# Performance work log

Hardware: AMD Instinct MI355X
Metric: run time of the kernel (lower is better)

## Reference

```python
import jax, jax.numpy as jnp
from jax import lax
import numpy as np

C = 256       # residual_channels == skip_channels
B = 4
T = 4096
LATENT = 128
NB = 4        # n_blocks
NL = 10       # n_layers
ENC_DILS = tuple(2 ** i for i in range(NL)) * NB   # 40 encoder blocks
DEC_DILS = tuple(2 ** i for i in range(NL))        # 10 decoder blocks


def causal_conv(x, W, b, d):
    # x: [B, Cin, T], W: [Cout, Cin, k], left-pad by (k-1)*d for causality
    pad = (W.shape[-1] - 1) * d
    y = lax.conv_general_dilated(x, W, (1,), [(pad, 0)], rhs_dilation=(d,),
                                 dimension_numbers=('NCH', 'OIH', 'NCH'))
    return y + b[None, :, None]


def gated_block(h, Wf, bf, Wg, bg, Wr, br, Ws, bs, d):
    f = jnp.tanh(causal_conv(h, Wf, bf, d))
    g = jax.nn.sigmoid(causal_conv(h, Wg, bg, d))
    out = f * g
    res = jnp.einsum('oc,bct->bot', Wr, out) + br[None, :, None] + h
    skip = jnp.einsum('oc,bct->bot', Ws, out) + bs[None, :, None]
    return res, skip


def setup_inputs() -> dict:
    key = jax.random.key(0)
    ks = jax.random.split(key, 24)
    s = 0.05
    nE = NB * NL
    d = {}
    d['x'] = jax.random.normal(ks[0], (B, 1, T), jnp.float32)
    d['eps'] = jax.random.normal(ks[1], (B, LATENT), jnp.float32)
    d['enc_in_W'] = jax.random.normal(ks[2], (C, 1, 2)) * s
    d['enc_in_b'] = jnp.zeros((C,), jnp.float32)
    d['enc_Wf'] = jax.random.normal(ks[3], (nE, C, C, 2)) * s
    d['enc_bf'] = jnp.zeros((nE, C), jnp.float32)
    d['enc_Wg'] = jax.random.normal(ks[4], (nE, C, C, 2)) * s
    d['enc_bg'] = jnp.zeros((nE, C), jnp.float32)
    d['enc_Wr'] = jax.random.normal(ks[5], (nE, C, C)) * s
    d['enc_br'] = jnp.zeros((nE, C), jnp.float32)
    d['enc_Ws'] = jax.random.normal(ks[6], (nE, C, C)) * s
    d['enc_bs'] = jnp.zeros((nE, C), jnp.float32)
    d['fc_mu_W'] = jax.random.normal(ks[7], (LATENT, C)) * s
    d['fc_mu_b'] = jnp.zeros((LATENT,), jnp.float32)
    d['fc_lv_W'] = jax.random.normal(ks[8], (LATENT, C)) * s
    d['fc_lv_b'] = jnp.zeros((LATENT,), jnp.float32)
    d['dec_in_W'] = jax.random.normal(ks[9], (C, LATENT)) * s
    d['dec_in_b'] = jnp.zeros((C,), jnp.float32)
    d['dec_Wf'] = jax.random.normal(ks[10], (NL, C, C, 2)) * s
    d['dec_bf'] = jnp.zeros((NL, C), jnp.float32)
    d['dec_Wg'] = jax.random.normal(ks[11], (NL, C, C, 2)) * s
    d['dec_bg'] = jnp.zeros((NL, C), jnp.float32)
    d['dec_Wr'] = jax.random.normal(ks[12], (NL, C, C)) * s
    d['dec_br'] = jnp.zeros((NL, C), jnp.float32)
    d['out_W'] = jax.random.normal(ks[13], (1, C)) * s
    d['out_b'] = jnp.zeros((1,), jnp.float32)
    return d


def _forward(x, eps, enc_in_W, enc_in_b, enc_Wf, enc_bf, enc_Wg, enc_bg,
             enc_Wr, enc_br, enc_Ws, enc_bs, fc_mu_W, fc_mu_b, fc_lv_W, fc_lv_b,
             dec_in_W, dec_in_b, dec_Wf, dec_bf, dec_Wg, dec_bg, dec_Wr, dec_br,
             out_W, out_b):
    # --- encode ---
    h = causal_conv(x, enc_in_W, enc_in_b, 1)
    skip_sum = jnp.zeros((h.shape[0], C, h.shape[2]), h.dtype)
    for i, dil in enumerate(ENC_DILS):
        h, skip = gated_block(h, enc_Wf[i], enc_bf[i], enc_Wg[i], enc_bg[i],
                              enc_Wr[i], enc_br[i], enc_Ws[i], enc_bs[i], dil)
        skip_sum = skip_sum + skip
    pooled = skip_sum.mean(axis=-1)                      # [B, C]
    mu = pooled @ fc_mu_W.T + fc_mu_b                    # [B, LATENT]
    logvar = pooled @ fc_lv_W.T + fc_lv_b
    # --- reparameterize ---
    z = mu + eps * jnp.exp(0.5 * logvar)
    # --- decode (length-1 sequence) ---
    h2 = (jnp.einsum('ol,bl->bo', dec_in_W, z) + dec_in_b)[:, :, None]  # [B, C, 1]
    for i, dil in enumerate(DEC_DILS):
        f = jnp.tanh(causal_conv(h2, dec_Wf[i], dec_bf[i], dil))
        g = jax.nn.sigmoid(causal_conv(h2, dec_Wg[i], dec_bg[i], dil))
        out = f * g
        h2 = jnp.einsum('oc,bct->bot', dec_Wr[i], out) + dec_br[i][None, :, None] + h2
    y = jnp.einsum('oc,bct->bot', out_W, h2) + out_b[None, :, None]     # [B, 1, 1]
    return (y, mu, logvar)


def reference(x, eps, enc_in_W, enc_in_b, enc_Wf, enc_bf, enc_Wg, enc_bg,
              enc_Wr, enc_br, enc_Ws, enc_bs, fc_mu_W, fc_mu_b, fc_lv_W, fc_lv_b,
              dec_in_W, dec_in_b, dec_Wf, dec_bf, dec_Wg, dec_bg, dec_Wr, dec_br,
              out_W, out_b):
    return _forward(x, eps, enc_in_W, enc_in_b, enc_Wf, enc_bf, enc_Wg, enc_bg,
                    enc_Wr, enc_br, enc_Ws, enc_bs, fc_mu_W, fc_mu_b, fc_lv_W, fc_lv_b,
                    dec_in_W, dec_in_b, dec_Wf, dec_bf, dec_Wg, dec_bg, dec_Wr, dec_br,
                    out_W, out_b)
```

## Files before the change

kernel.cpp:

```cpp
#include <hip/hip_runtime.h>

typedef unsigned short u16;
typedef __attribute__((ext_vector_type(8))) __bf16 bf16x8;
typedef __attribute__((ext_vector_type(4))) float f32x4;

constexpr int C = 256;
constexpr int T = 4096;
constexpr int B = 4;
constexpr int NENC = 40;
constexpr int NDEC = 10;
constexpr int TILE = 64;

__device__ __forceinline__ float bf2f(u16 v) {
  union { unsigned u; float f; } x;
  x.u = ((unsigned)v) << 16;
  return x.f;
}
__device__ __forceinline__ u16 f2bf(float f) {
  union { float ff; unsigned u; } x;
  x.ff = f;
  unsigned r = x.u + 0x7fffu + ((x.u >> 16) & 1u);
  return (u16)(r >> 16);
}
__device__ __forceinline__ int swz(int row, int col) {
  int g = ((row & 7) ^ (row >> 3)) & 7;
  return row * 512 + (col ^ (g << 3));
}

typedef __attribute__((address_space(1))) const unsigned int* gp1_t;
typedef __attribute__((address_space(3))) unsigned int* lp3_t;
__device__ __forceinline__ void gl_lds16(const u16* g, u16* l) {
  __builtin_amdgcn_global_load_lds((gp1_t)(const void*)g, (lp3_t)(void*)l, 16, 0, 0);
}

__global__ void k_pack1(const float* __restrict__ Wf, const float* __restrict__ Wg,
                        u16* __restrict__ penc1, int total) {
  int p = blockIdx.x * 256 + threadIdx.x;
  if (p >= total) return;
  int lane = p & 63;
  int s = (p >> 6) & 3;
  int c = (p >> 8) & 15;
  int wv = (p >> 12) & 7;
  int layer = p >> 15;
  int co = wv * 32 + (s & 1) * 16 + (lane & 15);
  int k = c * 32 + (lane >> 4) * 8;
  const float* src = (s >= 2 ? Wg : Wf) + ((size_t)layer * C + co) * 512 + k;
  u16* dst = penc1 + (size_t)p * 8;
#pragma unroll
  for (int r = 0; r < 8; ++r) dst[r] = f2bf(src[r]);
}

__global__ void k_pack2(const float* __restrict__ Wr, u16* __restrict__ penc2, int total) {
  int p = blockIdx.x * 256 + threadIdx.x;
  if (p >= total) return;
  int lane = p & 63;
  int s = (p >> 6) & 1;
  int c = (p >> 7) & 7;
  int wv = (p >> 10) & 7;
  int layer = p >> 13;
  int co = wv * 32 + s * 16 + (lane & 15);
  int k = c * 32 + (lane >> 4) * 8;
  const float* src = Wr + ((size_t)layer * C + co) * 256 + k;
  u16* dst = penc2 + (size_t)p * 8;
#pragma unroll
  for (int r = 0; r < 8; ++r) dst[r] = f2bf(src[r]);
}

__global__ void k_packd(const float* __restrict__ dWf, const float* __restrict__ dWg,
                        const float* __restrict__ dWr, const float* __restrict__ dinW,
                        u16* __restrict__ pdfg, u16* __restrict__ pdr,
                        u16* __restrict__ tdin) {
  int p = blockIdx.x * 256 + threadIdx.x;
  if (p < 163840) {
    int lane = p & 63;
    int s = (p >> 6) & 1;
    int c = (p >> 7) & 7;
    int wv = (p >> 10) & 15;
    int layer = p >> 14;
    int co = wv * 16 + (lane & 15);
    int k = c * 32 + (lane >> 4) * 8;
    const float* src = (s ? dWg : dWf) + (((size_t)(layer * C + co)) * C + k) * 2 + 1;
    u16* dst = pdfg + (size_t)p * 8;
#pragma unroll
    for (int r = 0; r < 8; ++r) dst[r] = f2bf(src[2 * r]);
  } else if (p < 245760) {
    int q = p - 163840;
    int lane = q & 63;
    int c = (q >> 6) & 7;
    int wv = (q >> 9) & 15;
    int layer = q >> 13;
    int co = wv * 16 + (lane & 15);
    int k = c * 32 + (lane >> 4) * 8;
    const float* src = dWr + ((size_t)(layer * C + co)) * C + k;
    u16* dst = pdr + (size_t)q * 8;
#pragma unroll
    for (int r = 0; r < 8; ++r) dst[r] = f2bf(src[r]);
  } else if (p < 249856) {
    int u = p - 245760;
#pragma unroll
    for (int r = 0; r < 8; ++r) tdin[u * 8 + r] = f2bf(dinW[u * 8 + r]);
  }
}

__global__ void k_zero(float* __restrict__ p, int n) {
  int i = blockIdx.x * 256 + threadIdx.x;
  if (i < n) p[i] = 0.f;
}

__global__ void k_input(const float* __restrict__ x, const float* __restrict__ W,
                        const float* __restrict__ bin, float* __restrict__ h) {
  int idx = blockIdx.x * 256 + threadIdx.x;
  int t = idx & (T - 1);
  int c = (idx >> 12) & (C - 1);
  int b = idx >> 20;
  float xv = x[b * T + t];
  float xp = (t > 0) ? x[b * T + t - 1] : 0.f;
  h[idx] = W[2 * c] * xp + W[2 * c + 1] * xv + bin[c];
}

__global__ __launch_bounds__(512, 2) void k_enc(
    const float* __restrict__ hin, float* __restrict__ hout, float* __restrict__ rowsum_l,
    const u16* __restrict__ pw1, const float* __restrict__ bfb,
    const float* __restrict__ bgb,
    const u16* __restrict__ pw2, const float* __restrict__ brb,
    int dil) {
  extern __shared__ __align__(16) u16 smem[];
  u16* wb = smem + 64 * 512;
  const int tid = threadIdx.x;
  const int wave = tid >> 6;
  const int lane = tid & 63;
  const int ncol = lane & 15;
  const int quad = lane >> 4;
  const int wg = blockIdx.x;
  const int b = wg >> 6;
  const int t0 = (wg & 63) * TILE;
  const float* hb = hin + b * C * T;

  const int co0 = wave * 32;
  const int kq = quad * 8;
  const u16* b1 = pw1 + wave * 32768 + lane * 8;
  const u16* b2 = pw2 + wave * 8192 + lane * 8;
  u16* wreg0 = wb + wave * 2048;
  u16* wreg1 = wb + 16384 + wave * 2048;
  const int aoff = lane * 8;

#pragma unroll
  for (int cc = 0; cc < 2; ++cc) {
    u16* ld = cc ? wreg1 : wreg0;
    gl_lds16(b1 + cc * 2048, ld);
    gl_lds16(b1 + cc * 2048 + 512, ld + 512);
    gl_lds16(b1 + cc * 2048 + 1024, ld + 1024);
    gl_lds16(b1 + cc * 2048 + 1536, ld + 1536);
  }

  const int n4 = tid & 15;
  const int cib = tid >> 4;
  float4 v[16];
  const bool al4 = ((dil & 3) == 0);
  if (t0 >= dil) {
#pragma unroll
    for (int it2 = 0; it2 < 16; ++it2) {
      int ci = (cib + it2 * 32) & 255;
      int tap = it2 >> 3;
      int tb = t0 + n4 * 4 - (tap ? 0 : dil);
      const float* p = hb + ci * T + tb;
      if (tap || al4) {
        v[it2] = *(const float4*)p;
      } else {
        v[it2].x = p[0]; v[it2].y = p[1]; v[it2].z = p[2]; v[it2].w = p[3];
      }
    }
  } else {
#pragma unroll
    for (int it2 = 0; it2 < 16; ++it2) {
      int ci = (cib + it2 * 32) & 255;
      int tap = it2 >> 3;
      int tb = t0 + n4 * 4 - (tap ? 0 : dil);
      const float* p = hb + ci * T + tb;
      if (tap) {
        v[it2] = *(const float4*)p;
      } else {
        v[it2].x = (tb + 0 >= 0) ? p[0] : 0.f;
        v[it2].y = (tb + 1 >= 0) ? p[1] : 0.f;
        v[it2].z = (tb + 2 >= 0) ? p[2] : 0.f;
        v[it2].w = (tb + 3 >= 0) ? p[3] : 0.f;
      }
    }
  }
#pragma unroll
  for (int it2 = 0; it2 < 8; ++it2) {
    int ci = (cib + it2 * 32) & 255;
    const float* p0 = (const float*)&v[it2];
    const float* p1 = (const float*)&v[it2 + 8];
#pragma unroll
    for (int r = 0; r < 4; ++r) {
      unsigned w32 = (unsigned)f2bf(p0[r]) | ((unsigned)f2bf(p1[r]) << 16);
      *(unsigned*)(&smem[swz(n4 * 4 + r, 2 * ci)]) = w32;
    }
  }
  __syncthreads();

  f32x4 acc[4][4];
#pragma unroll
  for (int m = 0; m < 4; ++m)
#pragma unroll
    for (int nt = 0; nt < 4; ++nt)
      acc[m][nt] = (f32x4){0.f, 0.f, 0.f, 0.f};

#pragma unroll
  for (int c = 0; c < 16; ++c) {
    if (c < 15) asm volatile("s_waitcnt vmcnt(4)" ::: "memory");
    else        asm volatile("s_waitcnt vmcnt(0)" ::: "memory");
    const u16* wr_ = (c & 1) ? wreg1 : wreg0;
    bf16x8 af0 = *(const bf16x8*)(wr_ + aoff);
    bf16x8 af1 = *(const bf16x8*)(wr_ + 512 + aoff);
    bf16x8 af2 = *(const bf16x8*)(wr_ + 1024 + aoff);
    bf16x8 af3 = *(const bf16x8*)(wr_ + 1536 + aoff);
    const int kk = c * 32 + kq;
    bf16x8 bfr[4];
#pragma unroll
    for (int nt = 0; nt < 4; ++nt)
      bfr[nt] = *(const bf16x8*)(&smem[swz(nt * 16 + ncol, kk)]);
#pragma unroll
    for (int nt = 0; nt < 4; ++nt) {
      acc[0][nt] = __builtin_amdgcn_mfma_f32_16x16x32_bf16(af0, bfr[nt], acc[0][nt], 0, 0, 0);
      acc[1][nt] = __builtin_amdgcn_mfma_f32_16x16x32_bf16(af1, bfr[nt], acc[1][nt], 0, 0, 0);
      acc[2][nt] = __builtin_amdgcn_mfma_f32_16x16x32_bf16(af2, bfr[nt], acc[2][nt], 0, 0, 0);
      acc[3][nt] = __builtin_amdgcn_mfma_f32_16x16x32_bf16(af3, bfr[nt], acc[3][nt], 0, 0, 0);
    }
    if (c + 2 < 16) {
      asm volatile("s_waitcnt lgkmcnt(0)" ::: "memory");
      u16* ld = (c & 1) ? wreg1 : wreg0;
      const u16* gs = b1 + (c + 2) * 2048;
      gl_lds16(gs, ld);
      gl_lds16(gs + 512, ld + 512);
      gl_lds16(gs + 1024, ld + 1024);
      gl_lds16(gs + 1536, ld + 1536);
    }
  }

#pragma unroll
  for (int cc = 0; cc < 2; ++cc) {
    u16* ld = cc ? wreg1 : wreg0;
    gl_lds16(b2 + cc * 1024, ld);
    gl_lds16(b2 + cc * 1024 + 512, ld + 512);
  }
  __syncthreads();

  float* rsb = rowsum_l + b * C;
#pragma unroll
  for (int j = 0; j < 2; ++j) {
    const int cob = co0 + j * 16 + quad * 4;
    float bfv[4], bgv[4], rs[4];
#pragma unroll
    for (int r = 0; r < 4; ++r) {
      bfv[r] = bfb[cob + r];
      bgv[r] = bgb[cob + r];
      rs[r] = 0.f;
    }
#pragma unroll
    for (int nt = 0; nt < 4; ++nt) {
      const int n = nt * 16 + ncol;
      u16 pk[4];
#pragma unroll
      for (int r = 0; r < 4; ++r) {
        float fv = acc[j][nt][r] + bfv[r];
        float gv = acc[2 + j][nt][r] + bgv[r];
        float th = 1.f - 2.f / (__expf(2.f * fv) + 1.f);
        float sg = 1.f / (1.f + __expf(-gv));
        float o = th * sg;
        rs[r] += o;
        pk[r] = f2bf(o);
      }
      uint2 w;
      w.x = (unsigned)pk[0] | ((unsigned)pk[1] << 16);
      w.y = (unsigned)pk[2] | ((unsigned)pk[3] << 16);
      *(uint2*)(&smem[swz(n, cob)]) = w;
    }
#pragma unroll
    for (int r = 0; r < 4; ++r) {
      float s = rs[r];
      s += __shfl_xor(s, 1);
      s += __shfl_xor(s, 2);
      s += __shfl_xor(s, 4);
      s += __shfl_xor(s, 8);
      if (ncol == 0) atomicAdd(&rsb[cob + r], s);
    }
  }
  __syncthreads();

  f32x4 acc2[2][4];
#pragma unroll
  for (int m = 0; m < 2; ++m)
#pragma unroll
    for (int nt = 0; nt < 4; ++nt)
      acc2[m][nt] = (f32x4){0.f, 0.f, 0.f, 0.f};

#pragma unroll
  for (int c = 0; c < 8; ++c) {
    if (c < 7) asm volatile("s_waitcnt vmcnt(2)" ::: "memory");
    else       asm volatile("s_waitcnt vmcnt(0)" ::: "memory");
    const u16* wr_ = (c & 1) ? wreg1 : wreg0;
    bf16x8 af0 = *(const bf16x8*)(wr_ + aoff);
    bf16x8 af1 = *(const bf16x8*)(wr_ + 512 + aoff);
    const int kk = c * 32 + kq;
    bf16x8 bfr[4];
#pragma unroll
    for (int nt = 0; nt < 4; ++nt)
      bfr[nt] = *(const bf16x8*)(&smem[swz(nt * 16 + ncol, kk)]);
#pragma unroll
    for (int nt = 0; nt < 4; ++nt) {
      acc2[0][nt] = __builtin_amdgcn_mfma_f32_16x16x32_bf16(af0, bfr[nt], acc2[0][nt], 0, 0, 0);
      acc2[1][nt] = __builtin_amdgcn_mfma_f32_16x16x32_bf16(af1, bfr[nt], acc2[1][nt], 0, 0, 0);
    }
    if (c + 2 < 8) {
      asm volatile("s_waitcnt lgkmcnt(0)" ::: "memory");
      u16* ld = (c & 1) ? wreg1 : wreg0;
      const u16* gs = b2 + (c + 2) * 1024;
      gl_lds16(gs, ld);
      gl_lds16(gs + 512, ld + 512);
    }
  }
  __syncthreads();

  float* fb = (float*)smem;
#pragma unroll
  for (int m = 0; m < 2; ++m) {
    const int cob = co0 + m * 16 + quad * 4;
#pragma unroll
    for (int nt = 0; nt < 4; ++nt) {
      const int t = nt * 16 + ncol;
#pragma unroll
      for (int r = 0; r < 4; ++r)
        fb[(cob + r) * 66 + t] = acc2[m][nt][r] + brb[cob + r];
    }
  }
  __syncthreads();
  float* ho = hout + b * C * T;
#pragma unroll
  for (int it2 = 0; it2 < 8; ++it2) {
    const int ci = cib + it2 * 32;
    const float* fr = fb + ci * 66 + n4 * 4;
    float4 o;
    o.x = fr[0] + v[it2 + 8].x;
    o.y = fr[1] + v[it2 + 8].y;
    o.z = fr[2] + v[it2 + 8].z;
    o.w = fr[3] + v[it2 + 8].w;
    *(float4*)(ho + ci * T + t0 + n4 * 4) = o;
  }
}

__global__ __launch_bounds__(256) void k_skip(
    const float* __restrict__ encWs, const float* __restrict__ encbs,
    const float* __restrict__ rowsum, float* __restrict__ pooled) {
  __shared__ float rs[B][C];
  const int l = blockIdx.x;
  const int co = threadIdx.x;
  for (int i = co; i < B * C; i += 256) rs[i >> 8][i & 255] = rowsum[l * B * C + i];
  __syncthreads();
  const float* Wrow = encWs + (size_t)l * C * C + co * C;
  float bs = encbs[l * C + co] * (float)T;
  float d[B] = {0.f, 0.f, 0.f, 0.f};
  for (int ci = 0; ci < C; ci += 4) {
    float4 w = *(const float4*)(Wrow + ci);
#pragma unroll
    for (int b = 0; b < B; ++b)
      d[b] += w.x * rs[b][ci] + w.y * rs[b][ci + 1] + w.z * rs[b][ci + 2] + w.w * rs[b][ci + 3];
  }
#pragma unroll
  for (int b = 0; b < B; ++b) atomicAdd(&pooled[b * C + co], d[b] + bs);
}

__global__ __launch_bounds__(256) void k_fc(
    const float* __restrict__ pooled,
    const float* __restrict__ muW, const float* __restrict__ mub,
    const float* __restrict__ lvW, const float* __restrict__ lvb,
    float* __restrict__ mlbuf, float* __restrict__ dout) {
  __shared__ float pm[B * C];
  const int tid = threadIdx.x;
  for (int i = tid; i < B * C; i += 256) pm[i] = pooled[i] * (1.f / (float)T);
  __syncthreads();
  const int waveG = blockIdx.x * 4 + (tid >> 6);
  const int lane = tid & 63;
  for (int j = 0; j < 16; ++j) {
    int d = waveG * 16 + j;
    int b = d >> 8, r = d & 255, which = r >> 7, l = r & 127;
    const float* Wrow = (which ? lvW : muW) + l * C;
    const float* p = pm + b * C;
    float s = Wrow[lane] * p[lane] + Wrow[lane + 64] * p[lane + 64] +
              Wrow[lane + 128] * p[lane + 128] + Wrow[lane + 192] * p[lane + 192];
#pragma unroll
    for (int off = 32; off; off >>= 1) s += __shfl_xor(s, off);
    if (lane == 0) {
      float val = s + (which ? lvb[l] : mub[l]);
      mlbuf[which * 512 + b * 128 + l] = val;
      dout[4 + which * 512 + b * 128 + l] = val;
    }
  }
}

__global__ __launch_bounds__(1024, 1) void k_dec(
    const float* __restrict__ mlbuf, const float* __restrict__ eps,
    const u16* __restrict__ tdin, const float* __restrict__ dinb,
    const u16* __restrict__ pdfg, const float* __restrict__ dbf,
    const float* __restrict__ dbg,
    const u16* __restrict__ pdr, const float* __restrict__ dbr,
    const float* __restrict__ outW, const float* __restrict__ outb,
    float* __restrict__ dout) {
  extern __shared__ __align__(16) u16 dsm[];
  __shared__ __align__(16) u16 Ah[16][264];
  __shared__ __align__(16) u16 Ao[16][264];
  __shared__ float h2f[4][256];
  __shared__ float outred[4];
  const int tid = threadIdx.x;
  const int wave = tid >> 6;
  const int lane = tid & 63;
  const int ncol = lane & 15;
  const int quad = lane >> 4;
  const int kq = quad * 8;
  const int co = wave * 16 + ncol;
  u16* wreg = dsm + wave * 4096;

  bf16x8 tdw[4];
  {
    const u16* wp = tdin + co * 128;
#pragma unroll
    for (int it = 0; it < 4; ++it) tdw[it] = *(const bf16x8*)(wp + it * 32 + kq);
  }

  if (tid < 512) {
    int b = tid >> 7, l = tid & 127;
    float mu = mlbuf[b * 128 + l];
    float lv = mlbuf[512 + b * 128 + l];
    Ah[b][l] = f2bf(mu + eps[b * 128 + l] * expf(0.5f * lv));
  }
  if (tid < 4) outred[tid] = 0.f;
  __syncthreads();

  {
    f32x4 acch = (f32x4){0.f, 0.f, 0.f, 0.f};
#pragma unroll
    for (int it = 0; it < 4; ++it) {
      bf16x8 af = *(const bf16x8*)(&Ah[ncol][it * 32 + kq]);
      acch = __builtin_amdgcn_mfma_f32_16x16x32_bf16(af, tdw[it], acch, 0, 0, 0);
    }
    __syncthreads();
    if (quad == 0) {
      float bias = dinb[co];
#pragma unroll
      for (int r = 0; r < 4; ++r) {
        float hv = acch[r] + bias;
        h2f[r][co] = hv;
        Ah[r][co] = f2bf(hv);
      }
    }
  }
  {
    const u16* fb = pdfg + wave * 8192 + lane * 8;
#pragma unroll
    for (int cc = 0; cc < 4; ++cc) {
      gl_lds16(fb + cc * 1024, wreg + cc * 1024);
      gl_lds16(fb + cc * 1024 + 512, wreg + cc * 1024 + 512);
    }
  }
  __syncthreads();

  for (int i = 0; i < NDEC; ++i) {
    const u16* fb = pdfg + (i * 16 + wave) * 8192 + lane * 8;
    const u16* rb = pdr + (i * 16 + wave) * 4096 + lane * 8;

    f32x4 accf = (f32x4){0.f, 0.f, 0.f, 0.f};
    f32x4 accg = (f32x4){0.f, 0.f, 0.f, 0.f};
#pragma unroll
    for (int c = 0; c < 8; ++c) {
      if (c == 4) asm volatile("s_waitcnt vmcnt(6)" ::: "memory");
      else if (c == 5) asm volatile("s_waitcnt vmcnt(4)" ::: "memory");
      else if (c == 6) asm volatile("s_waitcnt vmcnt(2)" ::: "memory");
      else if (c == 7) asm volatile("s_waitcnt vmcnt(0)" ::: "memory");
      const u16* bufp = wreg + (c & 3) * 1024;
      bf16x8 bf_ = *(const bf16x8*)(bufp + lane * 8);
      bf16x8 bg_ = *(const bf16x8*)(bufp + 512 + lane * 8);
      bf16x8 af = *(const bf16x8*)(&Ah[ncol][c * 32 + kq]);
      accf = __builtin_amdgcn_mfma_f32_16x16x32_bf16(af, bf_, accf, 0, 0, 0);
      accg = __builtin_amdgcn_mfma_f32_16x16x32_bf16(af, bg_, accg, 0, 0, 0);
      if (c < 4) {
        asm volatile("s_waitcnt lgkmcnt(0)" ::: "memory");
        gl_lds16(fb + (c + 4) * 1024, wreg + (c & 3) * 1024);
        gl_lds16(fb + (c + 4) * 1024 + 512, wreg + (c & 3) * 1024 + 512);
      }
    }
    asm volatile("s_waitcnt lgkmcnt(0)" ::: "memory");
#pragma unroll
    for (int cc = 0; cc < 4; ++cc) gl_lds16(rb + cc * 512, wreg + cc * 1024);

    if (quad == 0) {
      float bfv = dbf[i * C + co];
      float bgv = dbg[i * C + co];
#pragma unroll
      for (int r = 0; r < 4; ++r) {
        float fv = accf[r] + bfv;
        float gv = accg[r] + bgv;
        float th = 1.f - 2.f / (__expf(2.f * fv) + 1.f);
        float sg = 1.f / (1.f + __expf(-gv));
        Ao[r][co] = f2bf(th * sg);
      }
    }
    __syncthreads();

    f32x4 accr = (f32x4){0.f, 0.f, 0.f, 0.f};
#pragma unroll
    for (int c = 0; c < 8; ++c) {
      if (c == 4) asm volatile("s_waitcnt vmcnt(3)" ::: "memory");
      else if (c == 5) asm volatile("s_waitcnt vmcnt(2)" ::: "memory");
      else if (c == 6) asm volatile("s_waitcnt vmcnt(1)" ::: "memory");
      else if (c == 7) asm volatile("s_waitcnt vmcnt(0)" ::: "memory");
      bf16x8 br_ = *(const bf16x8*)(wreg + (c & 3) * 1024 + lane * 8);
      bf16x8 af = *(const bf16x8*)(&Ao[ncol][c * 32 + kq]);
      accr = __builtin_amdgcn_mfma_f32_16x16x32_bf16(af, br_, accr, 0, 0, 0);
      if (c < 4) {
        asm volatile("s_waitcnt lgkmcnt(0)" ::: "memory");
        gl_lds16(rb + (c + 4) * 512, wreg + (c & 3) * 1024);
      }
    }
    if (i + 1 < NDEC) {
      const u16* nfb = pdfg + ((i + 1) * 16 + wave) * 8192 + lane * 8;
      asm volatile("s_waitcnt lgkmcnt(0)" ::: "memory");
#pragma unroll
      for (int cc = 0; cc < 4; ++cc) {
        gl_lds16(nfb + cc * 1024, wreg + cc * 1024);
        gl_lds16(nfb + cc * 1024 + 512, wreg + cc * 1024 + 512);
      }
    }
    if (quad == 0) {
      float brv = dbr[i * C + co];
#pragma unroll
      for (int r = 0; r < 4; ++r) {
        float hv = h2f[r][co] + accr[r] + brv;
        h2f[r][co] = hv;
        Ah[r][co] = f2bf(hv);
      }
    }
    __syncthreads();
  }

  {
    int b = tid >> 8, c = tid & 255;
    float val = outW[c] * h2f[b][c];
#pragma unroll
    for (int off = 32; off; off >>= 1) val += __shfl_xor(val, off);
    if (lane == 0) atomicAdd(&outred[b], val);
  }
  __syncthreads();
  if (tid < 4) dout[tid] = outred[tid] + outb[0];
}

extern "C" void kernel_launch(void* const* d_in, const int* in_sizes, int n_in,
                              void* d_out, int out_size, void* d_ws, size_t ws_size,
                              hipStream_t stream) {
  const float* x      = (const float*)d_in[0];
  const float* eps    = (const float*)d_in[1];
  const float* encinW = (const float*)d_in[2];
  const float* encinb = (const float*)d_in[3];
  const float* encWf  = (const float*)d_in[4];
  const float* encbf  = (const float*)d_in[5];
  const float* encWg  = (const float*)d_in[6];
  const float* encbg  = (const float*)d_in[7];
  const float* encWr  = (const float*)d_in[8];
  const float* encbr  = (const float*)d_in[9];
  const float* encWs  = (const float*)d_in[10];
  const float* encbs  = (const float*)d_in[11];
  const float* muW    = (const float*)d_in[12];
  const float* mub    = (const float*)d_in[13];
  const float* lvW    = (const float*)d_in[14];
  const float* lvb    = (const float*)d_in[15];
  const float* dinW   = (const float*)d_in[16];
  const float* dinb   = (const float*)d_in[17];
  const float* dWf    = (const float*)d_in[18];
  const float* dbf    = (const float*)d_in[19];
  const float* dWg    = (const float*)d_in[20];
  const float* dbg    = (const float*)d_in[21];
  const float* dWr    = (const float*)d_in[22];
  const float* dbr    = (const float*)d_in[23];
  const float* outW   = (const float*)d_in[24];
  const float* outb   = (const float*)d_in[25];
  float* dout = (float*)d_out;

  char* ws = (char*)d_ws;
  float* hA = (float*)ws;
  float* hB = hA + (size_t)B * C * T;
  float* pooled = hB + (size_t)B * C * T;
  float* mlbuf = pooled + B * C;
  float* rowsum = mlbuf + 1024;
  u16* penc1 = (u16*)(rowsum + NENC * B * C);
  u16* penc2 = penc1 + (size_t)10485760;
  u16* pdfg = penc2 + (size_t)2621440;
  u16* pdr = pdfg + (size_t)1310720;
  u16* tdin = pdr + (size_t)655360;

  (void)hipFuncSetAttribute(reinterpret_cast<const void*>(k_enc),
                            hipFuncAttributeMaxDynamicSharedMemorySize, 131072);
  (void)hipFuncSetAttribute(reinterpret_cast<const void*>(k_dec),
                            hipFuncAttributeMaxDynamicSharedMemorySize, 131072);

  k_pack1<<<(1310720 + 255) / 256, 256, 0, stream>>>(encWf, encWg, penc1, 1310720);
  k_pack2<<<(327680 + 255) / 256, 256, 0, stream>>>(encWr, penc2, 327680);
  k_packd<<<(249856 + 255) / 256, 256, 0, stream>>>(dWf, dWg, dWr, dinW, pdfg, pdr, tdin);

  const int nZ = B * C + 1024 + NENC * B * C;
  k_zero<<<(nZ + 255) / 256, 256, 0, stream>>>(pooled, nZ);
  k_input<<<(B * C * T) / 256, 256, 0, stream>>>(x, encinW, encinb, hA);

  for (int i = 0; i < NENC; ++i) {
    const int dil = 1 << (i % 10);
    const float* hi = (i & 1) ? hB : hA;
    float* ho = (i & 1) ? hA : hB;
    k_enc<<<256, 512, 131072, stream>>>(
        hi, ho, rowsum + (size_t)i * B * C,
        penc1 + (size_t)i * 262144, encbf + (size_t)i * C,
        encbg + (size_t)i * C,
        penc2 + (size_t)i * 65536, encbr + (size_t)i * C,
        dil);
  }

  k_skip<<<NENC, 256, 0, stream>>>(encWs, encbs, rowsum, pooled);
  k_fc<<<16, 256, 0, stream>>>(pooled, muW, mub, lvW, lvb, mlbuf, dout);
  k_dec<<<1, 1024, 131072, stream>>>(mlbuf, eps, tdin, dinb, pdfg, dbf, dbg,
                                     pdr, dbr, outW, outb, dout);
}
```

Before: 1.279 ms.

## Use 1024-thread encoder blocks with 16 waves and triple-buffered weight streaming

Each encoder workgroup now runs 16 waves instead of 8, so every wave owns 16 output channels rather than 32. The weight packing layout is regenerated to match, and the per-wave weight staging moves from double to triple buffering in LDS. The activation tile is stored as half-width slabs, written in two phases with extra barriers partway through the K loop. This aims to raise latency hiding per CU and cut per-wave register pressure. The cost is more barriers and smaller per-wave MFMA tiles, which means less reuse of each B fragment.

```diff
diff --git a/kernel.cpp b/kernel.cpp
--- a/kernel.cpp
+++ b/kernel.cpp
@@ -22,9 +22,9 @@
   unsigned r = x.u + 0x7fffu + ((x.u >> 16) & 1u);
   return (u16)(r >> 16);
 }
-__device__ __forceinline__ int swz(int row, int col) {
+__device__ __forceinline__ int swz2(int row, int col) {
   int g = ((row & 7) ^ (row >> 3)) & 7;
-  return row * 512 + (col ^ (g << 3));
+  return row * 256 + (col ^ (g << 3));
 }
 
 typedef __attribute__((address_space(1))) const unsigned int* gp1_t;
@@ -38,13 +38,13 @@
   int p = blockIdx.x * 256 + threadIdx.x;
   if (p >= total) return;
   int lane = p & 63;
-  int s = (p >> 6) & 3;
-  int c = (p >> 8) & 15;
-  int wv = (p >> 12) & 7;
+  int s = (p >> 6) & 1;
+  int chunk = (p >> 7) & 15;
+  int w = (p >> 11) & 15;
   int layer = p >> 15;
-  int co = wv * 32 + (s & 1) * 16 + (lane & 15);
-  int k = c * 32 + (lane >> 4) * 8;
-  const float* src = (s >= 2 ? Wg : Wf) + ((size_t)layer * C + co) * 512 + k;
+  int co = w * 16 + (lane & 15);
+  int k = chunk * 32 + (lane >> 4) * 8;
+  const float* src = (s ? Wg : Wf) + ((size_t)layer * C + co) * 512 + k;
   u16* dst = penc1 + (size_t)p * 8;
 #pragma unroll
   for (int r = 0; r < 8; ++r) dst[r] = f2bf(src[r]);
@@ -54,12 +54,11 @@
   int p = blockIdx.x * 256 + threadIdx.x;
   if (p >= total) return;
   int lane = p & 63;
-  int s = (p >> 6) & 1;
-  int c = (p >> 7) & 7;
-  int wv = (p >> 10) & 7;
+  int chunk = (p >> 6) & 7;
+  int w = (p >> 9) & 15;
   int layer = p >> 13;
-  int co = wv * 32 + s * 16 + (lane & 15);
-  int k = c * 32 + (lane >> 4) * 8;
+  int co = w * 16 + (lane & 15);
+  int k = chunk * 32 + (lane >> 4) * 8;
   const float* src = Wr + ((size_t)layer * C + co) * 256 + k;
   u16* dst = penc2 + (size_t)p * 8;
 #pragma unroll
@@ -118,139 +117,129 @@
   h[idx] = W[2 * c] * xp + W[2 * c + 1] * xv + bin[c];
 }
 
-__global__ __launch_bounds__(512, 2) void k_enc(
+__global__ __launch_bounds__(1024, 1) void k_enc(
     const float* __restrict__ hin, float* __restrict__ hout, float* __restrict__ rowsum_l,
     const u16* __restrict__ pw1, const float* __restrict__ bfb,
     const float* __restrict__ bgb,
     const u16* __restrict__ pw2, const float* __restrict__ brb,
     int dil) {
   extern __shared__ __align__(16) u16 smem[];
-  u16* wb = smem + 64 * 512;
+  u16* wb = smem + 16384;
   const int tid = threadIdx.x;
   const int wave = tid >> 6;
   const int lane = tid & 63;
   const int ncol = lane & 15;
   const int quad = lane >> 4;
+  const int kq = quad * 8;
   const int wg = blockIdx.x;
   const int b = wg >> 6;
   const int t0 = (wg & 63) * TILE;
   const float* hb = hin + b * C * T;
 
-  const int co0 = wave * 32;
-  const int kq = quad * 8;
-  const u16* b1 = pw1 + wave * 32768 + lane * 8;
-  const u16* b2 = pw2 + wave * 8192 + lane * 8;
-  u16* wreg0 = wb + wave * 2048;
-  u16* wreg1 = wb + 16384 + wave * 2048;
-  const int aoff = lane * 8;
-
-#pragma unroll
-  for (int cc = 0; cc < 2; ++cc) {
-    u16* ld = cc ? wreg1 : wreg0;
-    gl_lds16(b1 + cc * 2048, ld);
-    gl_lds16(b1 + cc * 2048 + 512, ld + 512);
-    gl_lds16(b1 + cc * 2048 + 1024, ld + 1024);
-    gl_lds16(b1 + cc * 2048 + 1536, ld + 1536);
+  const u16* b1 = pw1 + wave * 16384 + lane * 8;
+  const u16* b2 = pw2 + wave * 4096 + lane * 8;
+  u16* wreg = wb + wave * 3072;
+
+#pragma unroll
+  for (int q = 0; q < 3; ++q) {
+    gl_lds16(b1 + q * 1024, wreg + q * 1024);
+    gl_lds16(b1 + q * 1024 + 512, wreg + q * 1024 + 512);
   }
 
   const int n4 = tid & 15;
-  const int cib = tid >> 4;
-  float4 v[16];
+  const int cib = (tid >> 4) & 63;
+  float4 v[8];
   const bool al4 = ((dil & 3) == 0);
   if (t0 >= dil) {
 #pragma unroll
-    for (int it2 = 0; it2 < 16; ++it2) {
-      int ci = (cib + it2 * 32) & 255;
-      int tap = it2 >> 3;
-      int tb = t0 + n4 * 4 - (tap ? 0 : dil);
-      const float* p = hb + ci * T + tb;
-      if (tap || al4) {
-        v[it2] = *(const float4*)p;
-      } else {
-        v[it2].x = p[0]; v[it2].y = p[1]; v[it2].z = p[2]; v[it2].w = p[3];
-      }
+    for (int j = 0; j < 4; ++j) {
+      int ci = cib + j * 64;
+      const float* p0 = hb + ci * T + t0 + n4 * 4 - dil;
+      if (al4) v[j] = *(const float4*)p0;
+      else { v[j].x = p0[0]; v[j].y = p0[1]; v[j].z = p0[2]; v[j].w = p0[3]; }
+      v[4 + j] = *(const float4*)(hb + ci * T + t0 + n4 * 4);
     }
   } else {
 #pragma unroll
-    for (int it2 = 0; it2 < 16; ++it2) {
-      int ci = (cib + it2 * 32) & 255;
-      int tap = it2 >> 3;
-      int tb = t0 + n4 * 4 - (tap ? 0 : dil);
-      const float* p = hb + ci * T + tb;
-      if (tap) {
-        v[it2] = *(const float4*)p;
-      } else {
-        v[it2].x = (tb + 0 >= 0) ? p[0] : 0.f;
-        v[it2].y = (tb + 1 >= 0) ? p[1] : 0.f;
-        v[it2].z = (tb + 2 >= 0) ? p[2] : 0.f;
-        v[it2].w = (tb + 3 >= 0) ? p[3] : 0.f;
-      }
-    }
-  }
-#pragma unroll
-  for (int it2 = 0; it2 < 8; ++it2) {
-    int ci = (cib + it2 * 32) & 255;
-    const float* p0 = (const float*)&v[it2];
-    const float* p1 = (const float*)&v[it2 + 8];
+    for (int j = 0; j < 4; ++j) {
+      int ci = cib + j * 64;
+      int tb = t0 + n4 * 4 - dil;
+      const float* p0 = hb + ci * T + tb;
+      v[j].x = (tb + 0 >= 0) ? p0[0] : 0.f;
+      v[j].y = (tb + 1 >= 0) ? p0[1] : 0.f;
+      v[j].z = (tb + 2 >= 0) ? p0[2] : 0.f;
+      v[j].w = (tb + 3 >= 0) ? p0[3] : 0.f;
+      v[4 + j] = *(const float4*)(hb + ci * T + t0 + n4 * 4);
+    }
+  }
+#pragma unroll
+  for (int j = 0; j < 2; ++j) {
+    int lc = 2 * cib + 128 * (j & 1);
+    const float* pa = (const float*)&v[j];
+    const float* pb = (const float*)&v[4 + j];
 #pragma unroll
     for (int r = 0; r < 4; ++r) {
-      unsigned w32 = (unsigned)f2bf(p0[r]) | ((unsigned)f2bf(p1[r]) << 16);
-      *(unsigned*)(&smem[swz(n4 * 4 + r, 2 * ci)]) = w32;
-    }
-  }
-  __syncthreads();
-
-  f32x4 acc[4][4];
-#pragma unroll
-  for (int m = 0; m < 4; ++m)
+      unsigned w32 = (unsigned)f2bf(pa[r]) | ((unsigned)f2bf(pb[r]) << 16);
+      *(unsigned*)(&smem[swz2(n4 * 4 + r, lc)]) = w32;
+    }
+  }
+  __syncthreads();
+
+  f32x4 accF[4], accG[4];
+#pragma unroll
+  for (int nt = 0; nt < 4; ++nt) {
+    accF[nt] = (f32x4){0.f, 0.f, 0.f, 0.f};
+    accG[nt] = (f32x4){0.f, 0.f, 0.f, 0.f};
+  }
+
+#pragma unroll
+  for (int gc = 0; gc < 16; ++gc) {
+    if (gc == 8) {
+      __syncthreads();
+#pragma unroll
+      for (int j = 2; j < 4; ++j) {
+        int lc = 2 * cib + 128 * (j & 1);
+        const float* pa = (const float*)&v[j];
+        const float* pb = (const float*)&v[4 + j];
+#pragma unroll
+        for (int r = 0; r < 4; ++r) {
+          unsigned w32 = (unsigned)f2bf(pa[r]) | ((unsigned)f2bf(pb[r]) << 16);
+          *(unsigned*)(&smem[swz2(n4 * 4 + r, lc)]) = w32;
+        }
+      }
+      __syncthreads();
+    }
+    if (gc <= 13)      asm volatile("s_waitcnt vmcnt(4)" ::: "memory");
+    else if (gc == 14) asm volatile("s_waitcnt vmcnt(2)" ::: "memory");
+    else               asm volatile("s_waitcnt vmcnt(0)" ::: "memory");
+    const u16* bufp = wreg + (gc % 3) * 1024;
+    bf16x8 af = *(const bf16x8*)(bufp + lane * 8);
+    bf16x8 ag = *(const bf16x8*)(bufp + 512 + lane * 8);
+    const int lc = (gc & 7) * 32 + kq;
+    bf16x8 bfr[4];
 #pragma unroll
     for (int nt = 0; nt < 4; ++nt)
-      acc[m][nt] = (f32x4){0.f, 0.f, 0.f, 0.f};
-
-#pragma unroll
-  for (int c = 0; c < 16; ++c) {
-    if (c < 15) asm volatile("s_waitcnt vmcnt(4)" ::: "memory");
-    else        asm volatile("s_waitcnt vmcnt(0)" ::: "memory");
-    const u16* wr_ = (c & 1) ? wreg1 : wreg0;
-    bf16x8 af0 = *(const bf16x8*)(wr_ + aoff);
-    bf16x8 af1 = *(const bf16x8*)(wr_ + 512 + aoff);
-    bf16x8 af2 = *(const bf16x8*)(wr_ + 1024 + aoff);
-    bf16x8 af3 = *(const bf16x8*)(wr_ + 1536 + aoff);
-    const int kk = c * 32 + kq;
-    bf16x8 bfr[4];
-#pragma unroll
-    for (int nt = 0; nt < 4; ++nt)
-      bfr[nt] = *(const bf16x8*)(&smem[swz(nt * 16 + ncol, kk)]);
+      bfr[nt] = *(const bf16x8*)(&smem[swz2(nt * 16 + ncol, lc)]);
 #pragma unroll
     for (int nt = 0; nt < 4; ++nt) {
-      acc[0][nt] = __builtin_amdgcn_mfma_f32_16x16x32_bf16(af0, bfr[nt], acc[0][nt], 0, 0, 0);
-      acc[1][nt] = __builtin_amdgcn_mfma_f32_16x16x32_bf16(af1, bfr[nt], acc[1][nt], 0, 0, 0);
-      acc[2][nt] = __builtin_amdgcn_mfma_f32_16x16x32_bf16(af2, bfr[nt], acc[2][nt], 0, 0, 0);
-      acc[3][nt] = __builtin_amdgcn_mfma_f32_16x16x32_bf16(af3, bfr[nt], acc[3][nt], 0, 0, 0);
-    }
-    if (c + 2 < 16) {
+      accF[nt] = __builtin_amdgcn_mfma_f32_16x16x32_bf16(af, bfr[nt], accF[nt], 0, 0, 0);
+      accG[nt] = __builtin_amdgcn_mfma_f32_16x16x32_bf16(ag, bfr[nt], accG[nt], 0, 0, 0);
+    }
+    if (gc + 3 < 16) {
       asm volatile("s_waitcnt lgkmcnt(0)" ::: "memory");
-      u16* ld = (c & 1) ? wreg1 : wreg0;
-      const u16* gs = b1 + (c + 2) * 2048;
-      gl_lds16(gs, ld);
-      gl_lds16(gs + 512, ld + 512);
-      gl_lds16(gs + 1024, ld + 1024);
-      gl_lds16(gs + 1536, ld + 1536);
-    }
-  }
-
-#pragma unroll
-  for (int cc = 0; cc < 2; ++cc) {
-    u16* ld = cc ? wreg1 : wreg0;
-    gl_lds16(b2 + cc * 1024, ld);
-    gl_lds16(b2 + cc * 1024 + 512, ld + 512);
-  }
+      u16* ld = wreg + (gc % 3) * 1024;
+      gl_lds16(b1 + (gc + 3) * 1024, ld);
+      gl_lds16(b1 + (gc + 3) * 1024 + 512, ld + 512);
+    }
+  }
+
+#pragma unroll
+  for (int q = 0; q < 3; ++q) gl_lds16(b2 + q * 512, wreg + q * 1024);
   __syncthreads();
 
   float* rsb = rowsum_l + b * C;
-#pragma unroll
-  for (int j = 0; j < 2; ++j) {
-    const int cob = co0 + j * 16 + quad * 4;
+  {
+    const int cob = wave * 16 + quad * 4;
     float bfv[4], bgv[4], rs[4];
 #pragma unroll
     for (int r = 0; r < 4; ++r) {
@@ -260,12 +249,12 @@
     }
 #pragma unroll
     for (int nt = 0; nt < 4; ++nt) {
-      const int n = nt * 16 + ncol;
+      const int t = nt * 16 + ncol;
       u16 pk[4];
 #pragma unroll
       for (int r = 0; r < 4; ++r) {
-        float fv = acc[j][nt][r] + bfv[r];
-        float gv = acc[2 + j][nt][r] + bgv[r];
+        float fv = accF[nt][r] + bfv[r];
+        float gv = accG[nt][r] + bgv[r];
         float th = 1.f - 2.f / (__expf(2.f * fv) + 1.f);
         float sg = 1.f / (1.f + __expf(-gv));
         float o = th * sg;
@@ -275,7 +264,7 @@
       uint2 w;
       w.x = (unsigned)pk[0] | ((unsigned)pk[1] << 16);
       w.y = (unsigned)pk[2] | ((unsigned)pk[3] << 16);
-      *(uint2*)(&smem[swz(n, cob)]) = w;
+      *(uint2*)(&smem[swz2(t, cob)]) = w;
     }
 #pragma unroll
     for (int r = 0; r < 4; ++r) {
@@ -289,63 +278,54 @@
   }
   __syncthreads();
 
-  f32x4 acc2[2][4];
-#pragma unroll
-  for (int m = 0; m < 2; ++m)
+  f32x4 accR[4];
+#pragma unroll
+  for (int nt = 0; nt < 4; ++nt) accR[nt] = (f32x4){0.f, 0.f, 0.f, 0.f};
+
+#pragma unroll
+  for (int c = 0; c < 8; ++c) {
+    if (c <= 5)      asm volatile("s_waitcnt vmcnt(2)" ::: "memory");
+    else if (c == 6) asm volatile("s_waitcnt vmcnt(1)" ::: "memory");
+    else             asm volatile("s_waitcnt vmcnt(0)" ::: "memory");
+    const u16* bufp = wreg + (c % 3) * 1024;
+    bf16x8 ar = *(const bf16x8*)(bufp + lane * 8);
+    const int lc = c * 32 + kq;
+    bf16x8 bfr[4];
 #pragma unroll
     for (int nt = 0; nt < 4; ++nt)
-      acc2[m][nt] = (f32x4){0.f, 0.f, 0.f, 0.f};
-
-#pragma unroll
-  for (int c = 0; c < 8; ++c) {
-    if (c < 7) asm volatile("s_waitcnt vmcnt(2)" ::: "memory");
-    else       asm volatile("s_waitcnt vmcnt(0)" ::: "memory");
-    const u16* wr_ = (c & 1) ? wreg1 : wreg0;
-    bf16x8 af0 = *(const bf16x8*)(wr_ + aoff);
-    bf16x8 af1 = *(const bf16x8*)(wr_ + 512 + aoff);
-    const int kk = c * 32 + kq;
-    bf16x8 bfr[4];
+      bfr[nt] = *(const bf16x8*)(&smem[swz2(nt * 16 + ncol, lc)]);
 #pragma unroll
     for (int nt = 0; nt < 4; ++nt)
-      bfr[nt] = *(const bf16x8*)(&smem[swz(nt * 16 + ncol, kk)]);
-#pragma unroll
-    for (int nt = 0; nt < 4; ++nt) {
-      acc2[0][nt] = __builtin_amdgcn_mfma_f32_16x16x32_bf16(af0, bfr[nt], acc2[0][nt], 0, 0, 0);
-      acc2[1][nt] = __builtin_amdgcn_mfma_f32_16x16x32_bf16(af1, bfr[nt], acc2[1][nt], 0, 0, 0);
-    }
-    if (c + 2 < 8) {
+      accR[nt] = __builtin_amdgcn_mfma_f32_16x16x32_bf16(ar, bfr[nt], accR[nt], 0, 0, 0);
+    if (c + 3 < 8) {
       asm volatile("s_waitcnt lgkmcnt(0)" ::: "memory");
-      u16* ld = (c & 1) ? wreg1 : wreg0;
-      const u16* gs = b2 + (c + 2) * 1024;
-      gl_lds16(gs, ld);
-      gl_lds16(gs + 512, ld + 512);
+      gl_lds16(b2 + (c + 3) * 512, wreg + (c % 3) * 1024);
     }
   }
   __syncthreads();
 
   float* fb = (float*)smem;
-#pragma unroll
-  for (int m = 0; m < 2; ++m) {
-    const int cob = co0 + m * 16 + quad * 4;
+  {
+    const int cob = wave * 16 + quad * 4;
 #pragma unroll
     for (int nt = 0; nt < 4; ++nt) {
       const int t = nt * 16 + ncol;
 #pragma unroll
       for (int r = 0; r < 4; ++r)
-        fb[(cob + r) * 66 + t] = acc2[m][nt][r] + brb[cob + r];
+        fb[(cob + r) * 66 + t] = accR[nt][r] + brb[cob + r];
     }
   }
   __syncthreads();
   float* ho = hout + b * C * T;
 #pragma unroll
-  for (int it2 = 0; it2 < 8; ++it2) {
-    const int ci = cib + it2 * 32;
+  for (int j = 0; j < 4; ++j) {
+    const int ci = cib + j * 64;
     const float* fr = fb + ci * 66 + n4 * 4;
     float4 o;
-    o.x = fr[0] + v[it2 + 8].x;
-    o.y = fr[1] + v[it2 + 8].y;
-    o.z = fr[2] + v[it2 + 8].z;
-    o.w = fr[3] + v[it2 + 8].w;
+    o.x = fr[0] + v[4 + j].x;
+    o.y = fr[1] + v[4 + j].y;
+    o.z = fr[2] + v[4 + j].z;
+    o.w = fr[3] + v[4 + j].w;
     *(float4*)(ho + ci * T + t0 + n4 * 4) = o;
   }
 }
@@ -614,7 +594,7 @@
     const int dil = 1 << (i % 10);
     const float* hi = (i & 1) ? hB : hA;
     float* ho = (i & 1) ? hA : hB;
-    k_enc<<<256, 512, 131072, stream>>>(
+    k_enc<<<256, 1024, 131072, stream>>>(
         hi, ho, rowsum + (size_t)i * B * C,
         penc1 + (size_t)i * 262144, encbf + (size_t)i * C,
         encbg + (size_t)i * C,
```

Measured after the change: 1.459 ms. 1.14x slower.

## Load encoder weights into registers, halve LDS, split decoder into chained launches

Applied to the files above, without the earlier changes.

The encoder kernel now prefetches A-operand weights straight from global memory into a 4-deep register ring instead of staging them through LDS with async copies. This cuts dynamic shared memory from 128KB to 64KB, and the output transpose is done in two halves so it fits. The goal is to raise occupancy and drop the LDS round-trip, at the cost of more registers and exposed global-load latency. The single-block decoder is also split into four chained launches that pass state through a global buffer. That split adds launch overhead and seems unrelated to speed.

```diff
diff --git a/kernel.cpp b/kernel.cpp
--- a/kernel.cpp
+++ b/kernel.cpp
@@ -125,32 +125,29 @@
     const u16* __restrict__ pw2, const float* __restrict__ brb,
     int dil) {
   extern __shared__ __align__(16) u16 smem[];
-  u16* wb = smem + 64 * 512;
   const int tid = threadIdx.x;
   const int wave = tid >> 6;
   const int lane = tid & 63;
   const int ncol = lane & 15;
   const int quad = lane >> 4;
+  const int kq = quad * 8;
   const int wg = blockIdx.x;
   const int b = wg >> 6;
   const int t0 = (wg & 63) * TILE;
   const float* hb = hin + b * C * T;
 
   const int co0 = wave * 32;
-  const int kq = quad * 8;
   const u16* b1 = pw1 + wave * 32768 + lane * 8;
   const u16* b2 = pw2 + wave * 8192 + lane * 8;
-  u16* wreg0 = wb + wave * 2048;
-  u16* wreg1 = wb + 16384 + wave * 2048;
-  const int aoff = lane * 8;
-
-#pragma unroll
-  for (int cc = 0; cc < 2; ++cc) {
-    u16* ld = cc ? wreg1 : wreg0;
-    gl_lds16(b1 + cc * 2048, ld);
-    gl_lds16(b1 + cc * 2048 + 512, ld + 512);
-    gl_lds16(b1 + cc * 2048 + 1024, ld + 1024);
-    gl_lds16(b1 + cc * 2048 + 1536, ld + 1536);
+
+  bf16x8 q0[4], q1[4], q2[4], q3[4];
+#pragma unroll
+  for (int p = 0; p < 4; ++p) {
+    const u16* gs = b1 + p * 2048;
+    q0[p] = *(const bf16x8*)(gs);
+    q1[p] = *(const bf16x8*)(gs + 512);
+    q2[p] = *(const bf16x8*)(gs + 1024);
+    q3[p] = *(const bf16x8*)(gs + 1536);
   }
 
   const int n4 = tid & 15;
@@ -209,13 +206,11 @@
 
 #pragma unroll
   for (int c = 0; c < 16; ++c) {
-    if (c < 15) asm volatile("s_waitcnt vmcnt(4)" ::: "memory");
-    else        asm volatile("s_waitcnt vmcnt(0)" ::: "memory");
-    const u16* wr_ = (c & 1) ? wreg1 : wreg0;
-    bf16x8 af0 = *(const bf16x8*)(wr_ + aoff);
-    bf16x8 af1 = *(const bf16x8*)(wr_ + 512 + aoff);
-    bf16x8 af2 = *(const bf16x8*)(wr_ + 1024 + aoff);
-    bf16x8 af3 = *(const bf16x8*)(wr_ + 1536 + aoff);
+    const int slot = c & 3;
+    bf16x8 af0 = q0[slot];
+    bf16x8 af1 = q1[slot];
+    bf16x8 af2 = q2[slot];
+    bf16x8 af3 = q3[slot];
     const int kk = c * 32 + kq;
     bf16x8 bfr[4];
 #pragma unroll
@@ -228,22 +223,21 @@
       acc[2][nt] = __builtin_amdgcn_mfma_f32_16x16x32_bf16(af2, bfr[nt], acc[2][nt], 0, 0, 0);
       acc[3][nt] = __builtin_amdgcn_mfma_f32_16x16x32_bf16(af3, bfr[nt], acc[3][nt], 0, 0, 0);
     }
-    if (c + 2 < 16) {
-      asm volatile("s_waitcnt lgkmcnt(0)" ::: "memory");
-      u16* ld = (c & 1) ? wreg1 : wreg0;
-      const u16* gs = b1 + (c + 2) * 2048;
-      gl_lds16(gs, ld);
-      gl_lds16(gs + 512, ld + 512);
-      gl_lds16(gs + 1024, ld + 1024);
-      gl_lds16(gs + 1536, ld + 1536);
-    }
-  }
-
-#pragma unroll
-  for (int cc = 0; cc < 2; ++cc) {
-    u16* ld = cc ? wreg1 : wreg0;
-    gl_lds16(b2 + cc * 1024, ld);
-    gl_lds16(b2 + cc * 1024 + 512, ld + 512);
+    if (c + 4 < 16) {
+      const u16* gs = b1 + (c + 4) * 2048;
+      q0[slot] = *(const bf16x8*)(gs);
+      q1[slot] = *(const bf16x8*)(gs + 512);
+      q2[slot] = *(const bf16x8*)(gs + 1024);
+      q3[slot] = *(const bf16x8*)(gs + 1536);
+    }
+  }
+
+  bf16x8 r0[4], r1[4];
+#pragma unroll
+  for (int p = 0; p < 4; ++p) {
+    const u16* gs = b2 + p * 1024;
+    r0[p] = *(const bf16x8*)(gs);
+    r1[p] = *(const bf16x8*)(gs + 512);
   }
   __syncthreads();
 
@@ -298,11 +292,9 @@
 
 #pragma unroll
   for (int c = 0; c < 8; ++c) {
-    if (c < 7) asm volatile("s_waitcnt vmcnt(2)" ::: "memory");
-    else       asm volatile("s_waitcnt vmcnt(0)" ::: "memory");
-    const u16* wr_ = (c & 1) ? wreg1 : wreg0;
-    bf16x8 af0 = *(const bf16x8*)(wr_ + aoff);
-    bf16x8 af1 = *(const bf16x8*)(wr_ + 512 + aoff);
+    const int slot = c & 3;
+    bf16x8 af0 = r0[slot];
+    bf16x8 af1 = r1[slot];
     const int kk = c * 32 + kq;
     bf16x8 bfr[4];
 #pragma unroll
@@ -313,40 +305,43 @@
       acc2[0][nt] = __builtin_amdgcn_mfma_f32_16x16x32_bf16(af0, bfr[nt], acc2[0][nt], 0, 0, 0);
       acc2[1][nt] = __builtin_amdgcn_mfma_f32_16x16x32_bf16(af1, bfr[nt], acc2[1][nt], 0, 0, 0);
     }
-    if (c + 2 < 8) {
-      asm volatile("s_waitcnt lgkmcnt(0)" ::: "memory");
-      u16* ld = (c & 1) ? wreg1 : wreg0;
-      const u16* gs = b2 + (c + 2) * 1024;
-      gl_lds16(gs, ld);
-      gl_lds16(gs + 512, ld + 512);
-    }
-  }
-  __syncthreads();
-
-  float* fb = (float*)smem;
-#pragma unroll
-  for (int m = 0; m < 2; ++m) {
-    const int cob = co0 + m * 16 + quad * 4;
-#pragma unroll
-    for (int nt = 0; nt < 4; ++nt) {
-      const int t = nt * 16 + ncol;
-#pragma unroll
-      for (int r = 0; r < 4; ++r)
-        fb[(cob + r) * 66 + t] = acc2[m][nt][r] + brb[cob + r];
-    }
-  }
-  __syncthreads();
+    if (c + 4 < 8) {
+      const u16* gs = b2 + (c + 4) * 1024;
+      r0[slot] = *(const bf16x8*)(gs);
+      r1[slot] = *(const bf16x8*)(gs + 512);
+    }
+  }
+
+  float* fbuf = (float*)smem;
   float* ho = hout + b * C * T;
 #pragma unroll
-  for (int it2 = 0; it2 < 8; ++it2) {
-    const int ci = cib + it2 * 32;
-    const float* fr = fb + ci * 66 + n4 * 4;
-    float4 o;
-    o.x = fr[0] + v[it2 + 8].x;
-    o.y = fr[1] + v[it2 + 8].y;
-    o.z = fr[2] + v[it2 + 8].z;
-    o.w = fr[3] + v[it2 + 8].w;
-    *(float4*)(ho + ci * T + t0 + n4 * 4) = o;
+  for (int h = 0; h < 2; ++h) {
+    __syncthreads();
+    if ((wave >> 2) == h) {
+#pragma unroll
+      for (int m = 0; m < 2; ++m) {
+        const int cob = co0 + m * 16 + quad * 4;
+#pragma unroll
+        for (int nt = 0; nt < 4; ++nt) {
+          const int t = nt * 16 + ncol;
+#pragma unroll
+          for (int r = 0; r < 4; ++r)
+            fbuf[(cob - 128 * h + r) * 66 + t] = acc2[m][nt][r] + brb[cob + r];
+        }
+      }
+    }
+    __syncthreads();
+#pragma unroll
+    for (int it2 = 4 * h; it2 < 4 * h + 4; ++it2) {
+      const int ci = cib + it2 * 32;
+      const float* fr = fbuf + (ci - 128 * h) * 66 + n4 * 4;
+      float4 o;
+      o.x = fr[0] + v[it2 + 8].x;
+      o.y = fr[1] + v[it2 + 8].y;
+      o.z = fr[2] + v[it2 + 8].z;
+      o.w = fr[3] + v[it2 + 8].w;
+      *(float4*)(ho + ci * T + t0 + n4 * 4) = o;
+    }
   }
 }
 
@@ -406,7 +401,8 @@
     const float* __restrict__ dbg,
     const u16* __restrict__ pdr, const float* __restrict__ dbr,
     const float* __restrict__ outW, const float* __restrict__ outb,
-    float* __restrict__ dout) {
+    float* __restrict__ gstate, float* __restrict__ dout,
+    int l0, int l1, int head, int tail) {
   extern __shared__ __align__(16) u16 dsm[];
   __shared__ __align__(16) u16 Ah[16][264];
   __shared__ __align__(16) u16 Ao[16][264];
@@ -421,23 +417,20 @@
   const int co = wave * 16 + ncol;
   u16* wreg = dsm + wave * 4096;
 
-  bf16x8 tdw[4];
-  {
-    const u16* wp = tdin + co * 128;
-#pragma unroll
-    for (int it = 0; it < 4; ++it) tdw[it] = *(const bf16x8*)(wp + it * 32 + kq);
-  }
-
-  if (tid < 512) {
-    int b = tid >> 7, l = tid & 127;
-    float mu = mlbuf[b * 128 + l];
-    float lv = mlbuf[512 + b * 128 + l];
-    Ah[b][l] = f2bf(mu + eps[b * 128 + l] * expf(0.5f * lv));
-  }
-  if (tid < 4) outred[tid] = 0.f;
-  __syncthreads();
-
-  {
+  if (head) {
+    bf16x8 tdw[4];
+    {
+      const u16* wp = tdin + co * 128;
+#pragma unroll
+      for (int it = 0; it < 4; ++it) tdw[it] = *(const bf16x8*)(wp + it * 32 + kq);
+    }
+    if (tid < 512) {
+      int b = tid >> 7, l = tid & 127;
+      float mu = mlbuf[b * 128 + l];
+      float lv = mlbuf[512 + b * 128 + l];
+      Ah[b][l] = f2bf(mu + eps[b * 128 + l] * expf(0.5f * lv));
+    }
+    __syncthreads();
     f32x4 acch = (f32x4){0.f, 0.f, 0.f, 0.f};
 #pragma unroll
     for (int it = 0; it < 4; ++it) {
@@ -454,9 +447,15 @@
         Ah[r][co] = f2bf(hv);
       }
     }
-  }
+  } else {
+    float hv = gstate[tid & 1023];
+    int b = (tid >> 8) & 3, c = tid & 255;
+    h2f[b][c] = hv;
+    Ah[b][c] = f2bf(hv);
+  }
+  if (tid < 4) outred[tid] = 0.f;
   {
-    const u16* fb = pdfg + wave * 8192 + lane * 8;
+    const u16* fb = pdfg + (l0 * 16 + wave) * 8192 + lane * 8;
 #pragma unroll
     for (int cc = 0; cc < 4; ++cc) {
       gl_lds16(fb + cc * 1024, wreg + cc * 1024);
@@ -465,7 +464,7 @@
   }
   __syncthreads();
 
-  for (int i = 0; i < NDEC; ++i) {
+  for (int i = l0; i < l1; ++i) {
     const u16* fb = pdfg + (i * 16 + wave) * 8192 + lane * 8;
     const u16* rb = pdr + (i * 16 + wave) * 4096 + lane * 8;
 
@@ -522,7 +521,7 @@
         gl_lds16(rb + (c + 4) * 512, wreg + (c & 3) * 1024);
       }
     }
-    if (i + 1 < NDEC) {
+    if (i + 1 < l1) {
       const u16* nfb = pdfg + ((i + 1) * 16 + wave) * 8192 + lane * 8;
       asm volatile("s_waitcnt lgkmcnt(0)" ::: "memory");
 #pragma unroll
@@ -543,15 +542,17 @@
     __syncthreads();
   }
 
-  {
+  if (tail) {
     int b = tid >> 8, c = tid & 255;
     float val = outW[c] * h2f[b][c];
 #pragma unroll
     for (int off = 32; off; off >>= 1) val += __shfl_xor(val, off);
     if (lane == 0) atomicAdd(&outred[b], val);
-  }
-  __syncthreads();
-  if (tid < 4) dout[tid] = outred[tid] + outb[0];
+    __syncthreads();
+    if (tid < 4) dout[tid] = outred[tid] + outb[0];
+  } else {
+    gstate[tid & 1023] = h2f[(tid >> 8) & 3][tid & 255];
+  }
 }
 
 extern "C" void kernel_launch(void* const* d_in, const int* in_sizes, int n_in,
@@ -591,14 +592,15 @@
   float* pooled = hB + (size_t)B * C * T;
   float* mlbuf = pooled + B * C;
   float* rowsum = mlbuf + 1024;
-  u16* penc1 = (u16*)(rowsum + NENC * B * C);
+  float* gstate = rowsum + NENC * B * C;
+  u16* penc1 = (u16*)(gstate + 1024);
   u16* penc2 = penc1 + (size_t)10485760;
   u16* pdfg = penc2 + (size_t)2621440;
   u16* pdr = pdfg + (size_t)1310720;
   u16* tdin = pdr + (size_t)655360;
 
   (void)hipFuncSetAttribute(reinterpret_cast<const void*>(k_enc),
-                            hipFuncAttributeMaxDynamicSharedMemorySize, 131072);
+                            hipFuncAttributeMaxDynamicSharedMemorySize, 65536);
   (void)hipFuncSetAttribute(reinterpret_cast<const void*>(k_dec),
                             hipFuncAttributeMaxDynamicSharedMemorySize, 131072);
 
@@ -614,7 +616,7 @@
     const int dil = 1 << (i % 10);
     const float* hi = (i & 1) ? hB : hA;
     float* ho = (i & 1) ? hA : hB;
-    k_enc<<<256, 512, 131072, stream>>>(
+    k_enc<<<256, 512, 65536, stream>>>(
         hi, ho, rowsum + (size_t)i * B * C,
         penc1 + (size_t)i * 262144, encbf + (size_t)i * C,
         encbg + (size_t)i * C,
@@ -625,5 +627,11 @@
   k_skip<<<NENC, 256, 0, stream>>>(encWs, encbs, rowsum, pooled);
   k_fc<<<16, 256, 0, stream>>>(pooled, muW, mub, lvW, lvb, mlbuf, dout);
   k_dec<<<1, 1024, 131072, stream>>>(mlbuf, eps, tdin, dinb, pdfg, dbf, dbg,
-                                     pdr, dbr, outW, outb, dout);
-}
+                                     pdr, dbr, outW, outb, gstate, dout, 0, 3, 1, 0);
+  k_dec<<<1, 1024, 131072, stream>>>(mlbuf, eps, tdin, dinb, pdfg, dbf, dbg,
+                                     pdr, dbr, outW, outb, gstate, dout, 3, 6, 0, 0);
+  k_dec<<<1, 1024, 131072, stream>>>(mlbuf, eps, tdin, dinb, pdfg, dbf, dbg,
+                                     pdr, dbr, outW, outb, gstate, dout, 6, 8, 0, 0);
+  k_dec<<<1, 1024, 131072, stream>>>(mlbuf, eps, tdin, dinb, pdfg, dbf, dbg,
+                                     pdr, dbr, outW, outb, gstate, dout, 8, 10, 0, 1);
+}
```

New measurement: 1.341 ms. 4.8% more time.
